# Kernel optimization log

Measured on AMD Instinct MI355X. Metric: run time of the kernel, lower is better.

The kernel has to match this reference:

```python
import jax, jax.numpy as jnp
import numpy as np

D_MODEL = 256
NHEAD = 8
NUM_LAYERS = 4
LN_EPS = 1e-5

def _layernorm(x, g, b):
    mu = jnp.mean(x, axis=-1, keepdims=True)
    var = jnp.mean((x - mu) ** 2, axis=-1, keepdims=True)
    return (x - mu) * jax.lax.rsqrt(var + LN_EPS) * g + b

def setup_inputs() -> dict:
    key = jax.random.key(0)
    ks = jax.random.split(key, 16)
    B, M, D, L = 2, 2048, D_MODEL, NUM_LAYERS
    s = 0.02
    inp = {
        'x': jax.random.normal(ks[0], (B, M, D), jnp.float32),
        'coords': jax.random.normal(ks[1], (B, M, 3), jnp.float32),
        'wq': jax.random.normal(ks[2], (L, D, D), jnp.float32) * s,
        'bq': jnp.zeros((L, D), jnp.float32),
        'wk': jax.random.normal(ks[3], (L, D, D), jnp.float32) * s,
        'bk': jnp.zeros((L, D), jnp.float32),
        'wv': jax.random.normal(ks[4], (L, D, D), jnp.float32) * s,
        'bv': jnp.zeros((L, D), jnp.float32),
        'alpha': jnp.full((L,), 0.1, jnp.float32),
        'w1': jax.random.normal(ks[5], (L, D, 2 * D), jnp.float32) * s,
        'b1': jnp.zeros((L, 2 * D), jnp.float32),
        'w2': jax.random.normal(ks[6], (L, 2 * D, D), jnp.float32) * s,
        'b2': jnp.zeros((L, D), jnp.float32),
        'ln1_g': jnp.ones((L, D), jnp.float32),
        'ln1_b': jnp.zeros((L, D), jnp.float32),
        'ln2_g': jnp.ones((L, D), jnp.float32),
        'ln2_b': jnp.zeros((L, D), jnp.float32),
    }
    return inp

def reference(x, coords, wq, bq, wk, bk, wv, bv, alpha, w1, b1, w2, b2, ln1_g, ln1_b, ln2_g, ln2_b):
    B, M, D = x.shape
    H = NHEAD
    dk = D // H
    # Geometric bias: per-batch block of the original B*M x B*M dot matrix,
    # i.e. G[b] = coords[b] @ coords[b].T  (identical math, computed directly).
    G0 = jnp.einsum('bmd,bnd->bmn', coords, coords)  # [B, M, M]
    scale = 1.0 / jnp.sqrt(jnp.asarray(dk, x.dtype))

    def heads(t):  # [B,M,D] -> [B,H,M,dk]
        return t.reshape(B, M, H, dk).transpose(0, 2, 1, 3)

    for i in range(NUM_LAYERS):
        q = heads(x @ wq[i] + bq[i])
        k = heads(x @ wk[i] + bk[i])
        v = heads(x @ wv[i] + bv[i])
        scores = jnp.einsum('bhmd,bhnd->bhmn', q, k) * scale + (alpha[i] * G0)[:, None]
        attn = jax.nn.softmax(scores, axis=-1)
        out = jnp.einsum('bhmn,bhnd->bhmd', attn, v)
        out = out.transpose(0, 2, 1, 3).reshape(B, M, D)
        x = _layernorm(x + out, ln1_g[i], ln1_b[i])
        ff = jax.nn.relu(x @ w1[i] + b1[i]) @ w2[i] + b2[i]
        x = _layernorm(x + ff, ln2_g[i], ln2_b[i])
    return x
```

## Files before the change

kernel.cpp:

```cpp
#include <hip/hip_runtime.h>

typedef unsigned short u16;
typedef __attribute__((ext_vector_type(8))) short short8;
typedef __attribute__((ext_vector_type(4))) float f32x4;
typedef __attribute__((ext_vector_type(4))) u16 u16x4;

#define MFMA16(a, b, c) __builtin_amdgcn_mfma_f32_16x16x32_bf16(a, b, c, 0, 0, 0)
#define EXP2(x) __builtin_amdgcn_exp2f(x)

#define LOG2E 1.4426950408889634f
#define QSCALE 0.25506038410312156f

__device__ __forceinline__ u16 f2bf(float f) {
    unsigned int u = __builtin_bit_cast(unsigned int, f);
    u += 0x7fffu + ((u >> 16) & 1u);
    return (u16)(u >> 16);
}

__global__ __launch_bounds__(256) void repack_kernel(
    const float* __restrict__ wq, const float* __restrict__ wk, const float* __restrict__ wv,
    const float* __restrict__ bq, const float* __restrict__ bk, const float* __restrict__ bv,
    const float* __restrict__ w1, const float* __restrict__ w2,
    u16* __restrict__ wqkvT, u16* __restrict__ w1T, u16* __restrict__ w2T,
    float* __restrict__ bqkv)
{
    long idx = (long)blockIdx.x * 256 + threadIdx.x;
    const long NQ = 4L * 768 * 256;
    const long N1 = 4L * 512 * 256;
    const long N2 = 4L * 256 * 512;
    const long NB = 4L * 768;
    if (idx < NQ) {
        long l = idx / (768 * 256); long r = idx % (768 * 256);
        long n = r / 256, k = r % 256;
        float v;
        if (n < 256)      v = wq[(l * 256 + k) * 256 + n] * QSCALE;
        else if (n < 512) v = wk[(l * 256 + k) * 256 + (n - 256)];
        else              v = wv[(l * 256 + k) * 256 + (n - 512)];
        wqkvT[idx] = f2bf(v);
    } else if ((idx -= NQ) < N1) {
        long l = idx / (512 * 256); long r = idx % (512 * 256);
        long n = r / 256, k = r % 256;
        w1T[idx] = f2bf(w1[(l * 256 + k) * 512 + n]);
    } else if ((idx -= N1) < N2) {
        long l = idx / (256 * 512); long r = idx % (256 * 512);
        long n = r / 512, k = r % 512;
        w2T[idx] = f2bf(w2[(l * 512 + k) * 256 + n]);
    } else if ((idx -= N2) < NB) {
        long l = idx / 768; long n = idx % 768;
        float v = (n < 256) ? bq[l * 256 + n] * QSCALE
                : (n < 512) ? bk[l * 256 + (n - 256)]
                            : bv[l * 256 + (n - 512)];
        bqkv[l * 768 + n] = v;
    }
}

__global__ __launch_bounds__(256) void xconv_kernel(
    const float* __restrict__ xin, const float* __restrict__ coords,
    float* __restrict__ xf, u16* __restrict__ xb, u16* __restrict__ kcoord)
{
    long idx = (long)blockIdx.x * 256 + threadIdx.x;
    if (idx < 4096L * 256) {
        float v = xin[idx];
        xf[idx] = v;
        xb[idx] = f2bf(v);
    }
    if (idx < 4096) {
        const float* c = coords + idx * 3;
        u16 r0 = f2bf(c[0] * LOG2E), r1 = f2bf(c[1] * LOG2E), r2 = f2bf(c[2] * LOG2E);
        uint4 lo; lo.x = (unsigned)r0 | ((unsigned)r1 << 16); lo.y = (unsigned)r2; lo.z = 0; lo.w = 0;
        uint4 z4; z4.x = 0; z4.y = 0; z4.z = 0; z4.w = 0;
        uint4* dst = (uint4*)(kcoord + idx * 32);
        dst[0] = lo; dst[1] = z4; dst[2] = z4; dst[3] = z4;
    }
}

__global__ __launch_bounds__(256) void qkvgemm_kernel(
    const u16* __restrict__ A, const u16* __restrict__ BT,
    const float* __restrict__ bias,
    u16* __restrict__ qt, u16* __restrict__ kt, u16* __restrict__ vt)
{
    const int K = 256;
    int w = threadIdx.x >> 6, lane = threadIdx.x & 63;
    int wr = w >> 1, wc = w & 1;
    int m0 = blockIdx.x * 64 + wr * 32;
    int n0 = blockIdx.y * 128 + wc * 64;
    int l16 = lane & 15, lhi = lane >> 4;

    f32x4 acc[2][4];
#pragma unroll
    for (int i = 0; i < 2; i++)
#pragma unroll
        for (int j = 0; j < 4; j++) acc[i][j] = (f32x4){0.f, 0.f, 0.f, 0.f};

    const u16* Ap = A + (size_t)(m0 + l16) * K + lhi * 8;
    const u16* Bp = BT + (size_t)(n0 + l16) * K + lhi * 8;

#pragma unroll 4
    for (int k = 0; k < K; k += 32) {
        short8 a0 = *(const short8*)(Ap + k);
        short8 a1 = *(const short8*)(Ap + (size_t)16 * K + k);
        short8 b[4];
#pragma unroll
        for (int j = 0; j < 4; j++) b[j] = *(const short8*)(Bp + (size_t)(j * 16) * K + k);
#pragma unroll
        for (int j = 0; j < 4; j++) {
            acc[0][j] = MFMA16(a0, b[j], acc[0][j]);
            acc[1][j] = MFMA16(a1, b[j], acc[1][j]);
        }
    }

#pragma unroll
    for (int i = 0; i < 2; i++)
#pragma unroll
        for (int j = 0; j < 4; j++) {
            int n = n0 + j * 16 + l16;
            float bs = bias[n];
            int sect = n >> 8;
            int h = (n >> 5) & 7;
            int d = n & 31;
            int m = m0 + i * 16 + lhi * 4;
            int b_ = m >> 11, mseq = m & 2047;
            if (sect < 2) {
                u16* dst = (sect == 0 ? qt : kt) + ((size_t)(b_ * 8 + h) * 2048 + mseq) * 32 + d;
#pragma unroll
                for (int r = 0; r < 4; r++) dst[(size_t)r * 32] = f2bf(acc[i][j][r] + bs);
            } else {
                u16x4 pk;
#pragma unroll
                for (int r = 0; r < 4; r++) pk[r] = f2bf(acc[i][j][r] + bs);
                *(u16x4*)(vt + ((size_t)(b_ * 8 + h) * 32 + d) * 2048 + mseq) = pk;
            }
        }
}

__global__ __launch_bounds__(256) void gemm_relu_kernel(
    const u16* __restrict__ A, const u16* __restrict__ BT,
    const float* __restrict__ bias, u16* __restrict__ outp,
    int M, int N, int K)
{
    int w = threadIdx.x >> 6, lane = threadIdx.x & 63;
    int wr = w >> 1, wc = w & 1;
    int m0 = blockIdx.x * 64 + wr * 32;
    int n0 = blockIdx.y * 128 + wc * 64;
    int l16 = lane & 15, lhi = lane >> 4;

    f32x4 acc[2][4];
#pragma unroll
    for (int i = 0; i < 2; i++)
#pragma unroll
        for (int j = 0; j < 4; j++) acc[i][j] = (f32x4){0.f, 0.f, 0.f, 0.f};

    const u16* Ap = A + (size_t)(m0 + l16) * K + lhi * 8;
    const u16* Bp = BT + (size_t)(n0 + l16) * K + lhi * 8;

#pragma unroll 4
    for (int k = 0; k < K; k += 32) {
        short8 a0 = *(const short8*)(Ap + k);
        short8 a1 = *(const short8*)(Ap + (size_t)16 * K + k);
        short8 b[4];
#pragma unroll
        for (int j = 0; j < 4; j++) b[j] = *(const short8*)(Bp + (size_t)(j * 16) * K + k);
#pragma unroll
        for (int j = 0; j < 4; j++) {
            acc[0][j] = MFMA16(a0, b[j], acc[0][j]);
            acc[1][j] = MFMA16(a1, b[j], acc[1][j]);
        }
    }

#pragma unroll
    for (int i = 0; i < 2; i++)
#pragma unroll
        for (int j = 0; j < 4; j++) {
            int n = n0 + j * 16 + l16;
            float bs = bias[n];
#pragma unroll
            for (int r = 0; r < 4; r++) {
                int m = m0 + i * 16 + lhi * 4 + r;
                outp[(size_t)m * N + n] = f2bf(fmaxf(acc[i][j][r] + bs, 0.f));
            }
        }
}

__global__ __launch_bounds__(256) void gemm_f32_kernel(
    const u16* __restrict__ A, const u16* __restrict__ BT,
    const float* __restrict__ bias, float* __restrict__ outp,
    int M, int N, int K)
{
    int w = threadIdx.x >> 6, lane = threadIdx.x & 63;
    int wr = w >> 1, wc = w & 1;
    int m0 = blockIdx.x * 64 + wr * 32;
    int n0 = blockIdx.y * 64 + wc * 32;
    int l16 = lane & 15, lhi = lane >> 4;

    f32x4 acc[2][2];
#pragma unroll
    for (int i = 0; i < 2; i++)
#pragma unroll
        for (int j = 0; j < 2; j++) acc[i][j] = (f32x4){0.f, 0.f, 0.f, 0.f};

    const u16* Ap = A + (size_t)(m0 + l16) * K + lhi * 8;
    const u16* Bp = BT + (size_t)(n0 + l16) * K + lhi * 8;

#pragma unroll 8
    for (int k = 0; k < K; k += 32) {
        short8 a0 = *(const short8*)(Ap + k);
        short8 a1 = *(const short8*)(Ap + (size_t)16 * K + k);
        short8 b0 = *(const short8*)(Bp + k);
        short8 b1 = *(const short8*)(Bp + (size_t)16 * K + k);
        acc[0][0] = MFMA16(a0, b0, acc[0][0]);
        acc[0][1] = MFMA16(a0, b1, acc[0][1]);
        acc[1][0] = MFMA16(a1, b0, acc[1][0]);
        acc[1][1] = MFMA16(a1, b1, acc[1][1]);
    }

#pragma unroll
    for (int i = 0; i < 2; i++)
#pragma unroll
        for (int j = 0; j < 2; j++) {
            int n = n0 + j * 16 + l16;
            float bs = bias[n];
#pragma unroll
            for (int r = 0; r < 4; r++) {
                int m = m0 + i * 16 + lhi * 4 + r;
                outp[(size_t)m * N + n] = acc[i][j][r] + bs;
            }
        }
}

__global__ __launch_bounds__(256, 2) void attn_kernel(
    const u16* __restrict__ qt, const u16* __restrict__ kt, const u16* __restrict__ vt,
    const u16* __restrict__ kcoord, const float* __restrict__ coords,
    const float* __restrict__ alpha, int layer,
    float* __restrict__ po, float* __restrict__ pml)
{
    int tid = threadIdx.x;
    int w = tid >> 6, lane = tid & 63;
    int flat = blockIdx.x;
    int bh = (flat & 7) | (((flat >> 3) & 1) << 3);
    int b = bh >> 3, h = bh & 7;
    int m0 = ((flat >> 4) & 63) * 32;
    int kvhalf = flat >> 10;
    int l16 = lane & 15, lhi = lane >> 4;

    __shared__ __align__(16) char smem[18432 + 1024];
    float* olds = (float*)smem;
    float* mlds = (float*)(smem + 18432);
    u16* plbase = (u16*)smem;

    const u16* qbase = qt + (size_t)bh * 2048 * 32;
    float al = alpha[layer];
    short8 qlo[2], qhi[2];
#pragma unroll
    for (int qq = 0; qq < 2; qq++) {
        qlo[qq] = *(const short8*)(qbase + (size_t)(m0 + qq * 16 + l16) * 32 + lhi * 8);
        short8 z = {0, 0, 0, 0, 0, 0, 0, 0};
        qhi[qq] = z;
        if (lhi == 0) {
            const float* c = coords + (size_t)(b * 2048 + m0 + qq * 16 + l16) * 3;
            qhi[qq][0] = (short)f2bf(c[0] * al);
            qhi[qq][1] = (short)f2bf(c[1] * al);
            qhi[qq][2] = (short)f2bf(c[2] * al);
        }
    }

    f32x4 oacc[2][2];
#pragma unroll
    for (int qq = 0; qq < 2; qq++)
#pragma unroll
        for (int dt = 0; dt < 2; dt++) oacc[qq][dt] = (f32x4){0.f, 0.f, 0.f, 0.f};
    float mrow[2] = {-1e30f, -1e30f}, lrow[2] = {0.f, 0.f};

    int nbase = kvhalf * 16 + w * 4;
    int nstart = nbase * 64;

    unsigned kidx = ((unsigned)(bh * 2048 + nstart + l16) << 5) + lhi * 8;
    unsigned cidx = ((unsigned)(b * 2048 + nstart + l16) << 5) + lhi * 8;
    unsigned vidxA = ((unsigned)(bh * 32 + l16) << 11) + nstart + lhi * 8;
    unsigned vidxB = vidxA + (16u << 11);

    int hb = lhi >> 1, s7 = l16 & 7, lo4 = (lhi & 1) * 4;
    int wb = w * 2048 + l16 * 64;
    int wa[4], ra[2];
#pragma unroll
    for (int t = 0; t < 4; t++) wa[t] = wb + (((((t << 1) | hb)) ^ s7) << 3) + lo4;
#pragma unroll
    for (int kk = 0; kk < 2; kk++) ra[kk] = wb + ((((kk << 2) | lhi) ^ s7) << 3);

    short8 klo[2][4];
#pragma unroll
    for (int t = 0; t < 4; t++) klo[0][t] = *(const short8*)(kt + kidx + t * 512);
    kidx += 2048;

#pragma unroll
    for (int nbi = 0; nbi < 4; nbi++) {
        const int cur = nbi & 1, nxt = cur ^ 1;
        if (nbi < 3) {
#pragma unroll
            for (int t = 0; t < 4; t++) klo[nxt][t] = *(const short8*)(kt + kidx + t * 512);
            kidx += 2048;
        }
        short8 khi[4];
#pragma unroll
        for (int t = 0; t < 4; t++) khi[t] = *(const short8*)(kcoord + cidx + t * 512);
        cidx += 2048;
        short8 v0a = *(const short8*)(vt + vidxA);
        short8 v0b = *(const short8*)(vt + vidxA + 32);
        short8 v1a = *(const short8*)(vt + vidxB);
        short8 v1b = *(const short8*)(vt + vidxB + 32);
        vidxA += 64; vidxB += 64;

        f32x4 s[2][4];
#pragma unroll
        for (int t = 0; t < 4; t++) {
            f32x4 z0 = (f32x4){0.f, 0.f, 0.f, 0.f};
            z0 = MFMA16(klo[cur][t], qlo[0], z0);
            s[0][t] = MFMA16(khi[t], qhi[0], z0);
            f32x4 z1 = (f32x4){0.f, 0.f, 0.f, 0.f};
            z1 = MFMA16(klo[cur][t], qlo[1], z1);
            s[1][t] = MFMA16(khi[t], qhi[1], z1);
        }
#pragma unroll
        for (int qq = 0; qq < 2; qq++) {
            float lm = -1e30f;
#pragma unroll
            for (int t = 0; t < 4; t++) {
                float a = fmaxf(fmaxf(s[qq][t][0], s[qq][t][1]), fmaxf(s[qq][t][2], s[qq][t][3]));
                lm = fmaxf(lm, a);
            }
            if (!__all(lm <= mrow[qq] + 8.f)) {
                float tm = fmaxf(lm, __shfl_xor(lm, 16, 64));
                tm = fmaxf(tm, __shfl_xor(tm, 32, 64));
                float mnew = fmaxf(mrow[qq], tm);
                float corr = EXP2(mrow[qq] - mnew);
                mrow[qq] = mnew;
#pragma unroll
                for (int dt = 0; dt < 2; dt++)
#pragma unroll
                    for (int r = 0; r < 4; r++) oacc[qq][dt][r] *= corr;
                lrow[qq] *= corr;
            }

            float rs = 0.f;
#pragma unroll
            for (int t = 0; t < 4; t++) {
#pragma unroll
                for (int r = 0; r < 4; r++) s[qq][t][r] = EXP2(s[qq][t][r] - mrow[qq]);
                rs += (s[qq][t][0] + s[qq][t][1]) + (s[qq][t][2] + s[qq][t][3]);
            }
            lrow[qq] += rs;

            u16* pl = plbase + qq * 1024;
#pragma unroll
            for (int t = 0; t < 4; t++) {
                unsigned p0, p1;
                asm("v_cvt_pk_bf16_f32 %0, %1, %2" : "=v"(p0) : "v"(s[qq][t][0]), "v"(s[qq][t][1]));
                asm("v_cvt_pk_bf16_f32 %0, %1, %2" : "=v"(p1) : "v"(s[qq][t][2]), "v"(s[qq][t][3]));
                uint2 val; val.x = p0; val.y = p1;
                *(uint2*)(pl + wa[t]) = val;
            }
        }

        {
            short8 pf0 = *(const short8*)(plbase + ra[0]);
            short8 pf1 = *(const short8*)(plbase + 1024 + ra[0]);
            oacc[0][0] = MFMA16(v0a, pf0, oacc[0][0]);
            oacc[1][0] = MFMA16(v0a, pf1, oacc[1][0]);
            oacc[0][1] = MFMA16(v1a, pf0, oacc[0][1]);
            oacc[1][1] = MFMA16(v1a, pf1, oacc[1][1]);
        }
        {
            short8 pf0 = *(const short8*)(plbase + ra[1]);
            short8 pf1 = *(const short8*)(plbase + 1024 + ra[1]);
            oacc[0][0] = MFMA16(v0b, pf0, oacc[0][0]);
            oacc[1][0] = MFMA16(v0b, pf1, oacc[1][0]);
            oacc[0][1] = MFMA16(v1b, pf0, oacc[0][1]);
            oacc[1][1] = MFMA16(v1b, pf1, oacc[1][1]);
        }
    }

#pragma unroll
    for (int qq = 0; qq < 2; qq++) {
        lrow[qq] += __shfl_xor(lrow[qq], 16, 64);
        lrow[qq] += __shfl_xor(lrow[qq], 32, 64);
    }

    __syncthreads();
    if (lhi == 0) {
#pragma unroll
        for (int qq = 0; qq < 2; qq++) {
            mlds[((w * 2 + qq) * 2 + 0) * 16 + l16] = mrow[qq];
            mlds[((w * 2 + qq) * 2 + 1) * 16 + l16] = lrow[qq];
        }
    }
#pragma unroll
    for (int qq = 0; qq < 2; qq++)
#pragma unroll
        for (int dt = 0; dt < 2; dt++)
            *(f32x4*)(olds + ((size_t)(w * 2 + qq) * 16 + l16) * 36 + dt * 16 + lhi * 4) = oacc[qq][dt];
    __syncthreads();

    int d = tid & 31, q8 = tid >> 5;
#pragma unroll
    for (int qq2 = 0; qq2 < 4; qq2++) {
        int q = q8 + qq2 * 8;
        int q16 = q & 15, qh2 = q >> 4;
        float mw[4], lw[4];
#pragma unroll
        for (int ww = 0; ww < 4; ww++) {
            mw[ww] = mlds[((ww * 2 + qh2) * 2 + 0) * 16 + q16];
            lw[ww] = mlds[((ww * 2 + qh2) * 2 + 1) * 16 + q16];
        }
        float mg = fmaxf(fmaxf(mw[0], mw[1]), fmaxf(mw[2], mw[3]));
        float o = 0.f, lg = 0.f;
#pragma unroll
        for (int ww = 0; ww < 4; ww++) {
            float sc = EXP2(mw[ww] - mg);
            lg += lw[ww] * sc;
            o += olds[((size_t)(ww * 2 + qh2) * 16 + q16) * 36 + d] * sc;
        }
        size_t row = (size_t)(b * 2048 + m0 + q);
        po[((size_t)kvhalf * 4096 + row) * 256 + h * 32 + d] = o;
        if (d == 0) {
            float2 ml2; ml2.x = mg; ml2.y = lg;
            *(float2*)(pml + ((size_t)kvhalf * 4096 + row) * 16 + h * 2) = ml2;
        }
    }
}

__global__ __launch_bounds__(256) void lnmerge_kernel(
    const float* __restrict__ xin, const float* __restrict__ po,
    const float* __restrict__ pml,
    const float* __restrict__ g, const float* __restrict__ bb,
    float* __restrict__ outf, u16* __restrict__ outb)
{
    int w = threadIdx.x >> 6, lane = threadIdx.x & 63;
    int row = blockIdx.x * 4 + w;
    int h = lane >> 3;
    float m0v = pml[(size_t)row * 16 + h * 2];
    float l0v = pml[(size_t)row * 16 + h * 2 + 1];
    float m1v = pml[((size_t)4096 + row) * 16 + h * 2];
    float l1v = pml[((size_t)4096 + row) * 16 + h * 2 + 1];
    float mg = fmaxf(m0v, m1v);
    float w0 = exp2f(m0v - mg), w1 = exp2f(m1v - mg);
    float inv = 1.f / (l0v * w0 + l1v * w1);

    size_t base = (size_t)row * 256 + lane * 4;
    float4 xv = *(const float4*)(xin + base);
    float4 a0 = *(const float4*)(po + base);
    float4 a1 = *(const float4*)(po + (size_t)4096 * 256 + base);
    float s0 = xv.x + (a0.x * w0 + a1.x * w1) * inv;
    float s1 = xv.y + (a0.y * w0 + a1.y * w1) * inv;
    float s2 = xv.z + (a0.z * w0 + a1.z * w1) * inv;
    float s3 = xv.w + (a0.w * w0 + a1.w * w1) * inv;

    float sum = s0 + s1 + s2 + s3;
    float sq = s0 * s0 + s1 * s1 + s2 * s2 + s3 * s3;
#pragma unroll
    for (int off = 1; off < 64; off <<= 1) {
        sum += __shfl_xor(sum, off, 64);
        sq += __shfl_xor(sq, off, 64);
    }
    float mu = sum * (1.f / 256.f);
    float var = sq * (1.f / 256.f) - mu * mu;
    float rs = rsqrtf(var + 1e-5f);
    float4 gv = *(const float4*)(g + lane * 4);
    float4 bv = *(const float4*)(bb + lane * 4);
    float y0 = (s0 - mu) * rs * gv.x + bv.x;
    float y1 = (s1 - mu) * rs * gv.y + bv.y;
    float y2 = (s2 - mu) * rs * gv.z + bv.z;
    float y3 = (s3 - mu) * rs * gv.w + bv.w;
    float4 yo; yo.x = y0; yo.y = y1; yo.z = y2; yo.w = y3;
    *(float4*)(outf + base) = yo;
    unsigned int p0 = (unsigned int)f2bf(y0) | ((unsigned int)f2bf(y1) << 16);
    unsigned int p1 = (unsigned int)f2bf(y2) | ((unsigned int)f2bf(y3) << 16);
    uint2 pk; pk.x = p0; pk.y = p1;
    *(uint2*)(outb + base) = pk;
}

__global__ __launch_bounds__(256) void ln_kernel(
    const float* __restrict__ xin, const float* __restrict__ add,
    const float* __restrict__ g, const float* __restrict__ bb,
    float* __restrict__ outf, u16* __restrict__ outb)
{
    int w = threadIdx.x >> 6, lane = threadIdx.x & 63;
    int row = blockIdx.x * 4 + w;
    size_t base = (size_t)row * 256 + lane * 4;
    float4 xv = *(const float4*)(xin + base);
    float4 av = *(const float4*)(add + base);
    float s0 = xv.x + av.x, s1 = xv.y + av.y, s2 = xv.z + av.z, s3 = xv.w + av.w;
    float sum = s0 + s1 + s2 + s3;
    float sq = s0 * s0 + s1 * s1 + s2 * s2 + s3 * s3;
#pragma unroll
    for (int off = 1; off < 64; off <<= 1) {
        sum += __shfl_xor(sum, off, 64);
        sq += __shfl_xor(sq, off, 64);
    }
    float mu = sum * (1.f / 256.f);
    float var = sq * (1.f / 256.f) - mu * mu;
    float rs = rsqrtf(var + 1e-5f);
    float4 gv = *(const float4*)(g + lane * 4);
    float4 bv = *(const float4*)(bb + lane * 4);
    float y0 = (s0 - mu) * rs * gv.x + bv.x;
    float y1 = (s1 - mu) * rs * gv.y + bv.y;
    float y2 = (s2 - mu) * rs * gv.z + bv.z;
    float y3 = (s3 - mu) * rs * gv.w + bv.w;
    float4 yo; yo.x = y0; yo.y = y1; yo.z = y2; yo.w = y3;
    *(float4*)(outf + base) = yo;
    unsigned int p0 = (unsigned int)f2bf(y0) | ((unsigned int)f2bf(y1) << 16);
    unsigned int p1 = (unsigned int)f2bf(y2) | ((unsigned int)f2bf(y3) << 16);
    uint2 pk; pk.x = p0; pk.y = p1;
    *(uint2*)(outb + base) = pk;
}

extern "C" void kernel_launch(void* const* d_in, const int* in_sizes, int n_in,
                              void* d_out, int out_size, void* d_ws, size_t ws_size,
                              hipStream_t stream)
{
    const float* x_in   = (const float*)d_in[0];
    const float* coords = (const float*)d_in[1];
    const float* wq = (const float*)d_in[2];
    const float* bq = (const float*)d_in[3];
    const float* wk = (const float*)d_in[4];
    const float* bk = (const float*)d_in[5];
    const float* wv = (const float*)d_in[6];
    const float* bv = (const float*)d_in[7];
    const float* alpha = (const float*)d_in[8];
    const float* w1 = (const float*)d_in[9];
    const float* b1 = (const float*)d_in[10];
    const float* w2 = (const float*)d_in[11];
    const float* b2 = (const float*)d_in[12];
    const float* ln1g = (const float*)d_in[13];
    const float* ln1b = (const float*)d_in[14];
    const float* ln2g = (const float*)d_in[15];
    const float* ln2b = (const float*)d_in[16];
    float* out = (float*)d_out;

    char* ws = (char*)d_ws;
    size_t off = 0;
    auto alloc = [&](size_t bytes) -> void* {
        void* p = ws + off;
        off += (bytes + 255) & ~(size_t)255;
        return p;
    };
    float* x_f32 = (float*)alloc(4096UL * 256 * 4);
    u16*   x_bf  = (u16*)  alloc(4096UL * 256 * 2);
    u16*   qt    = (u16*)  alloc(16UL * 2048 * 32 * 2);
    u16*   ktp   = (u16*)  alloc(16UL * 2048 * 32 * 2);
    u16*   vtp   = (u16*)  alloc(16UL * 32 * 2048 * 2);
    u16*   kcoord= (u16*)  alloc(2UL * 2048 * 32 * 2);
    float* po    = (float*)alloc(2UL * 4096 * 256 * 4);
    float* pml   = (float*)alloc(2UL * 4096 * 16 * 4);
    u16*   mid   = (u16*)  alloc(4096UL * 512 * 2);
    float* ffn   = (float*)alloc(4096UL * 256 * 4);
    u16*   wqkvT = (u16*)  alloc(4UL * 768 * 256 * 2);
    u16*   w1T   = (u16*)  alloc(4UL * 512 * 256 * 2);
    u16*   w2T   = (u16*)  alloc(4UL * 256 * 512 * 2);
    float* bqkv  = (float*)alloc(4UL * 768 * 4);

    repack_kernel<<<7180, 256, 0, stream>>>(wq, wk, wv, bq, bk, bv, w1, w2,
                                            wqkvT, w1T, w2T, bqkv);
    xconv_kernel<<<4096, 256, 0, stream>>>(x_in, coords, x_f32, x_bf, kcoord);

    for (int i = 0; i < 4; i++) {
        qkvgemm_kernel<<<dim3(64, 6), 256, 0, stream>>>(
            x_bf, wqkvT + (size_t)i * 768 * 256, bqkv + i * 768, qt, ktp, vtp);
        attn_kernel<<<2048, 256, 0, stream>>>(qt, ktp, vtp, kcoord, coords, alpha, i, po, pml);
        lnmerge_kernel<<<1024, 256, 0, stream>>>(x_f32, po, pml, ln1g + i * 256, ln1b + i * 256,
                                                 x_f32, x_bf);
        gemm_relu_kernel<<<dim3(64, 4), 256, 0, stream>>>(
            x_bf, w1T + (size_t)i * 512 * 256, b1 + i * 512, mid, 4096, 512, 256);
        gemm_f32_kernel<<<dim3(64, 4), 256, 0, stream>>>(
            mid, w2T + (size_t)i * 256 * 512, b2 + i * 256, ffn, 4096, 256, 512);
        ln_kernel<<<1024, 256, 0, stream>>>(x_f32, ffn, ln2g + i * 256, ln2b + i * 256,
                                            (i == 3) ? out : x_f32, x_bf);
    }
}
```

Before: 323.1 us.

## Double-buffer K, coord and V tile loads with inline asm and explicit waitcnt

Replaces compiler-scheduled global loads in the attention kernel with inline-asm global_load_dwordx4 issued one tile ahead for K, key-coordinate and V data. Explicit s_waitcnt vmcnt counts and a scheduling barrier let the next tile's loads stay in flight while the current tile computes. Before, only K was prefetched and the coord and V loads were issued in the same iteration that used them. This raises register pressure because three double buffers are held, and correctness now depends on the manual vmcnt bookkeeping.

```diff
diff --git a/kernel.cpp b/kernel.cpp
--- a/kernel.cpp
+++ b/kernel.cpp
@@ -10,6 +10,9 @@
 
 #define LOG2E 1.4426950408889634f
 #define QSCALE 0.25506038410312156f
+
+#define GL(dst, p, o) asm volatile("global_load_dwordx4 %0, %1, off offset:" #o \
+                                   : "=v"(dst) : "v"(p))
 
 __device__ __forceinline__ u16 f2bf(float f) {
     unsigned int u = __builtin_bit_cast(unsigned int, f);
@@ -250,9 +253,10 @@
     const u16* qbase = qt + (size_t)bh * 2048 * 32;
     float al = alpha[layer];
     short8 qlo[2], qhi[2];
+    GL(qlo[0], (qbase + (size_t)(m0 + l16) * 32 + lhi * 8), 0);
+    GL(qlo[1], (qbase + (size_t)(m0 + 16 + l16) * 32 + lhi * 8), 0);
 #pragma unroll
     for (int qq = 0; qq < 2; qq++) {
-        qlo[qq] = *(const short8*)(qbase + (size_t)(m0 + qq * 16 + l16) * 32 + lhi * 8);
         short8 z = {0, 0, 0, 0, 0, 0, 0, 0};
         qhi[qq] = z;
         if (lhi == 0) {
@@ -262,6 +266,7 @@
             qhi[qq][2] = (short)f2bf(c[2] * al);
         }
     }
+    asm volatile("s_waitcnt vmcnt(0)" ::: "memory");
 
     f32x4 oacc[2][2];
 #pragma unroll
@@ -270,13 +275,12 @@
         for (int dt = 0; dt < 2; dt++) oacc[qq][dt] = (f32x4){0.f, 0.f, 0.f, 0.f};
     float mrow[2] = {-1e30f, -1e30f}, lrow[2] = {0.f, 0.f};
 
-    int nbase = kvhalf * 16 + w * 4;
-    int nstart = nbase * 64;
-
-    unsigned kidx = ((unsigned)(bh * 2048 + nstart + l16) << 5) + lhi * 8;
-    unsigned cidx = ((unsigned)(b * 2048 + nstart + l16) << 5) + lhi * 8;
-    unsigned vidxA = ((unsigned)(bh * 32 + l16) << 11) + nstart + lhi * 8;
-    unsigned vidxB = vidxA + (16u << 11);
+    int nstart = (kvhalf * 16 + w * 4) * 64;
+
+    const u16* pK  = kt + ((size_t)(bh * 2048 + nstart + l16) << 5) + lhi * 8;
+    const u16* pC  = kcoord + ((size_t)(b * 2048 + nstart + l16) << 5) + lhi * 8;
+    const u16* pVa = vt + ((size_t)(bh * 32 + l16) << 11) + nstart + lhi * 8;
+    const u16* pVb = pVa + ((size_t)16 << 11);
 
     int hb = lhi >> 1, s7 = l16 & 7, lo4 = (lhi & 1) * 4;
     int wb = w * 2048 + l16 * 64;
@@ -286,38 +290,36 @@
 #pragma unroll
     for (int kk = 0; kk < 2; kk++) ra[kk] = wb + ((((kk << 2) | lhi) ^ s7) << 3);
 
-    short8 klo[2][4];
-#pragma unroll
-    for (int t = 0; t < 4; t++) klo[0][t] = *(const short8*)(kt + kidx + t * 512);
-    kidx += 2048;
+    short8 bK[2][4], bC[2][4], bV[2][4];
+
+#define ISSUE_TILE(B)                                                     \
+    GL(bK[B][0], pK, 0);   GL(bK[B][1], pK, 1024);                        \
+    GL(bK[B][2], pK, 2048); GL(bK[B][3], pK, 3072);                       \
+    GL(bC[B][0], pC, 0);   GL(bC[B][1], pC, 1024);                        \
+    GL(bC[B][2], pC, 2048); GL(bC[B][3], pC, 3072);                       \
+    GL(bV[B][0], pVa, 0);  GL(bV[B][1], pVa, 64);                         \
+    GL(bV[B][2], pVb, 0);  GL(bV[B][3], pVb, 64);                         \
+    pK += 2048; pC += 2048; pVa += 64; pVb += 64;
+
+    ISSUE_TILE(0)
 
 #pragma unroll
     for (int nbi = 0; nbi < 4; nbi++) {
         const int cur = nbi & 1, nxt = cur ^ 1;
-        if (nbi < 3) {
-#pragma unroll
-            for (int t = 0; t < 4; t++) klo[nxt][t] = *(const short8*)(kt + kidx + t * 512);
-            kidx += 2048;
-        }
-        short8 khi[4];
-#pragma unroll
-        for (int t = 0; t < 4; t++) khi[t] = *(const short8*)(kcoord + cidx + t * 512);
-        cidx += 2048;
-        short8 v0a = *(const short8*)(vt + vidxA);
-        short8 v0b = *(const short8*)(vt + vidxA + 32);
-        short8 v1a = *(const short8*)(vt + vidxB);
-        short8 v1b = *(const short8*)(vt + vidxB + 32);
-        vidxA += 64; vidxB += 64;
+        if (nbi < 3) { ISSUE_TILE(nxt) }
+        if (nbi < 3) asm volatile("s_waitcnt vmcnt(12)" ::: "memory");
+        else         asm volatile("s_waitcnt vmcnt(0)" ::: "memory");
+        __builtin_amdgcn_sched_barrier(0);
 
         f32x4 s[2][4];
 #pragma unroll
         for (int t = 0; t < 4; t++) {
             f32x4 z0 = (f32x4){0.f, 0.f, 0.f, 0.f};
-            z0 = MFMA16(klo[cur][t], qlo[0], z0);
-            s[0][t] = MFMA16(khi[t], qhi[0], z0);
+            z0 = MFMA16(bK[cur][t], qlo[0], z0);
+            s[0][t] = MFMA16(bC[cur][t], qhi[0], z0);
             f32x4 z1 = (f32x4){0.f, 0.f, 0.f, 0.f};
-            z1 = MFMA16(klo[cur][t], qlo[1], z1);
-            s[1][t] = MFMA16(khi[t], qhi[1], z1);
+            z1 = MFMA16(bK[cur][t], qlo[1], z1);
+            s[1][t] = MFMA16(bC[cur][t], qhi[1], z1);
         }
 #pragma unroll
         for (int qq = 0; qq < 2; qq++) {
@@ -363,20 +365,21 @@
         {
             short8 pf0 = *(const short8*)(plbase + ra[0]);
             short8 pf1 = *(const short8*)(plbase + 1024 + ra[0]);
-            oacc[0][0] = MFMA16(v0a, pf0, oacc[0][0]);
-            oacc[1][0] = MFMA16(v0a, pf1, oacc[1][0]);
-            oacc[0][1] = MFMA16(v1a, pf0, oacc[0][1]);
-            oacc[1][1] = MFMA16(v1a, pf1, oacc[1][1]);
+            oacc[0][0] = MFMA16(bV[cur][0], pf0, oacc[0][0]);
+            oacc[1][0] = MFMA16(bV[cur][0], pf1, oacc[1][0]);
+            oacc[0][1] = MFMA16(bV[cur][2], pf0, oacc[0][1]);
+            oacc[1][1] = MFMA16(bV[cur][2], pf1, oacc[1][1]);
         }
         {
             short8 pf0 = *(const short8*)(plbase + ra[1]);
             short8 pf1 = *(const short8*)(plbase + 1024 + ra[1]);
-            oacc[0][0] = MFMA16(v0b, pf0, oacc[0][0]);
-            oacc[1][0] = MFMA16(v0b, pf1, oacc[1][0]);
-            oacc[0][1] = MFMA16(v1b, pf0, oacc[0][1]);
-            oacc[1][1] = MFMA16(v1b, pf1, oacc[1][1]);
-        }
-    }
+            oacc[0][0] = MFMA16(bV[cur][1], pf0, oacc[0][0]);
+            oacc[1][0] = MFMA16(bV[cur][1], pf1, oacc[1][0]);
+            oacc[0][1] = MFMA16(bV[cur][3], pf0, oacc[0][1]);
+            oacc[1][1] = MFMA16(bV[cur][3], pf1, oacc[1][1]);
+        }
+    }
+#undef ISSUE_TILE
 
 #pragma unroll
     for (int qq = 0; qq < 2; qq++) {
```

Measured after the change: 324.0 us. About the same (+0.3%).
